# Kernel tuning notes

Measured on AMD Instinct MI355X. Metric: run time of the kernel, lower is better.

## Reference

```python
import jax, jax.numpy as jnp
import numpy as np

B, L, C, H, W = 2, 8, 64, 128, 128
HID = 256


def setup_inputs() -> dict:
    key = jax.random.key(0)
    k0, k1, k2, k3, k4 = jax.random.split(key, 5)
    x = jax.random.normal(k0, (B, L, C, H, W), dtype=jnp.float32)
    # Conv2d(in*4 -> hidden, kernel=1): weight stored as [out, in] for 1x1
    conv_w = jax.random.normal(k1, (HID, 4 * C), dtype=jnp.float32) * (1.0 / np.sqrt(4 * C))
    conv_b = jax.random.normal(k2, (HID,), dtype=jnp.float32) * 0.01
    conv_out_w = jax.random.normal(k3, (4 * C, HID), dtype=jnp.float32) * (1.0 / np.sqrt(HID))
    conv_out_b = jax.random.normal(k4, (4 * C,), dtype=jnp.float32) * 0.01
    return {"x": x, "conv_w": conv_w, "conv_b": conv_b,
            "conv_out_w": conv_out_w, "conv_out_b": conv_out_b}


def _dwt(x):  # x: [N, C, Hp, Wp] (even dims) -> [N, 4C, Hp/2, Wp/2]
    x1 = x[:, :, 0::2, 0::2] * 0.5
    x2 = x[:, :, 1::2, 0::2] * 0.5
    x3 = x[:, :, 0::2, 1::2] * 0.5
    x4 = x[:, :, 1::2, 1::2] * 0.5
    return jnp.concatenate([x1 + x2 + x3 + x4,
                            -x1 - x2 + x3 + x4,
                            -x1 + x2 - x3 + x4,
                            x1 - x2 - x3 + x4], axis=1)


def _idwt(y):  # y: [N, 4C, Hh, Wh] -> [N, C, 2Hh, 2Wh]
    n, c4, hh, wh = y.shape
    co = c4 // 4
    y1 = y[:, 0 * co:1 * co] * 0.5
    y2 = y[:, 1 * co:2 * co] * 0.5
    y3 = y[:, 2 * co:3 * co] * 0.5
    y4 = y[:, 3 * co:4 * co] * 0.5
    a = y1 - y2 - y3 + y4   # h[0::2, 0::2]
    b = y1 - y2 + y3 - y4   # h[1::2, 0::2]
    c = y1 + y2 - y3 - y4   # h[0::2, 1::2]
    d = y1 + y2 + y3 + y4   # h[1::2, 1::2]
    r0 = jnp.stack([a, c], axis=-1).reshape(n, co, hh, 2 * wh)  # even rows
    r1 = jnp.stack([b, d], axis=-1).reshape(n, co, hh, 2 * wh)  # odd rows
    return jnp.stack([r0, r1], axis=-2).reshape(n, co, 2 * hh, 2 * wh)


def reference(x, conv_w, conv_b, conv_out_w, conv_out_b):
    b, l, c, h, w = x.shape
    pad_h = (2 - h % 2) % 2
    pad_w = (2 - w % 2) % 2
    if pad_h > 0 or pad_w > 0:
        x = jnp.pad(x, ((0, 0), (0, 0), (0, 0), (0, pad_h), (0, pad_w)))
    hp, wp = x.shape[-2], x.shape[-1]
    xf = x.reshape(b * l, c, hp, wp)
    x_dwt = _dwt(xf)                                       # [BL, 4C, hp/2, wp/2]
    feat = jnp.einsum('nchw,oc->nohw', x_dwt, conv_w) + conv_b[None, :, None, None]
    feat = jax.nn.silu(feat)
    y = jnp.einsum('nchw,oc->nohw', feat, conv_out_w) + conv_out_b[None, :, None, None]
    rec = _idwt(y)                                         # [BL, C, hp, wp]
    out = rec.reshape(b, l, c, hp, wp)
    if pad_h > 0 or pad_w > 0:
        out = out[..., :h, :w]
    return out
```

## Files before the change

### kernel.cpp

```cpp
#include <hip/hip_runtime.h>
#include <hip/hip_bf16.h>


typedef __bf16 bf16x8 __attribute__((ext_vector_type(8)));
typedef float  f32x4  __attribute__((ext_vector_type(4)));

#define SP 264

__device__ __forceinline__ unsigned short f2bf(float f) {
  __hip_bfloat16 h = __float2bfloat16(f);
  return __builtin_bit_cast(unsigned short, h);
}
__device__ __forceinline__ float bf2f(unsigned short s) {
  union { unsigned int i; float f; } v; v.i = ((unsigned int)s) << 16; return v.f;
}
__device__ __forceinline__ float silu(float f) {
  return f / (1.0f + __expf(-f));
}
__device__ __forceinline__ bf16x8 ldw8(const float* __restrict__ p) {
  const float4 a = *(const float4*)p;
  const float4 b = *(const float4*)(p + 4);
  bf16x8 r;
  r[0] = (__bf16)a.x; r[1] = (__bf16)a.y; r[2] = (__bf16)a.z; r[3] = (__bf16)a.w;
  r[4] = (__bf16)b.x; r[5] = (__bf16)b.y; r[6] = (__bf16)b.z; r[7] = (__bf16)b.w;
  return r;
}

__global__ __launch_bounds__(256) void cvt_w(const float* __restrict__ w1,
                                             const float* __restrict__ w2,
                                             unsigned short* __restrict__ o) {
  const int i = (blockIdx.x * 256 + threadIdx.x) * 4;
  const float4 a = *(const float4*)(w1 + i);
  const float4 b = *(const float4*)(w2 + i);
  *(ushort4*)(o + i)         = make_ushort4(f2bf(a.x), f2bf(a.y), f2bf(a.z), f2bf(a.w));
  *(ushort4*)(o + 65536 + i) = make_ushort4(f2bf(b.x), f2bf(b.y), f2bf(b.z), f2bf(b.w));
}

template <bool WBF16>
__global__ __launch_bounds__(256, 4)
void wavelet_fused(const float* __restrict__ x,
                   const void* __restrict__ w1p,
                   const float* __restrict__ b1,
                   const void* __restrict__ w2p,
                   const float* __restrict__ b2,
                   float* __restrict__ out)
{
  __shared__ unsigned short lds[64 * SP];

  const int t  = threadIdx.x;
  const int n  = blockIdx.x >> 6;
  const int hh = blockIdx.x & 63;

  const int ww = t & 63;
  const int cg = t >> 6;

  {
    const float* xb = x + ((size_t)n * 64 * 128 + (size_t)(2 * hh)) * 128 + 2 * ww;
    #pragma unroll
    for (int j = 0; j < 4; ++j) {
      const int c0 = (cg + 4 * j) * 4;
      float qv[4][4];
      #pragma unroll
      for (int ci = 0; ci < 4; ++ci) {
        const float* p = xb + (size_t)(c0 + ci) * (128 * 128);
        const float2 r0 = *(const float2*)p;
        const float2 r1 = *(const float2*)(p + 128);
        const float x1 = r0.x, x3 = r0.y;
        const float x2 = r1.x, x4 = r1.y;
        qv[0][ci] = 0.5f * ((x1 + x2) + (x3 + x4));
        qv[1][ci] = 0.5f * ((x3 + x4) - (x1 + x2));
        qv[2][ci] = 0.5f * ((x2 + x4) - (x1 + x3));
        qv[3][ci] = 0.5f * ((x1 + x4) - (x2 + x3));
      }
      #pragma unroll
      for (int q = 0; q < 4; ++q) {
        ushort4 v = make_ushort4(f2bf(qv[q][0]), f2bf(qv[q][1]), f2bf(qv[q][2]), f2bf(qv[q][3]));
        *(ushort4*)(&lds[ww * SP + q * 64 + c0]) = v;
      }
    }
  }
  __syncthreads();

  const int wv   = t >> 6;
  const int r    = t & 15;
  const int quad = (t & 63) >> 4;

  {
    f32x4 acc[4][4];
    #pragma unroll
    for (int mt = 0; mt < 4; ++mt)
      #pragma unroll
      for (int nt = 0; nt < 4; ++nt)
        acc[mt][nt] = (f32x4){0.0f, 0.0f, 0.0f, 0.0f};

    #pragma unroll
    for (int k0 = 0; k0 < 256; k0 += 32) {
      bf16x8 a[4], b[4];
      #pragma unroll
      for (int mt = 0; mt < 4; ++mt) {
        const int row = wv * 64 + mt * 16 + r;
        if constexpr (WBF16)
          a[mt] = *(const bf16x8*)((const unsigned short*)w1p + row * 256 + quad * 8 + k0);
        else
          a[mt] = ldw8((const float*)w1p + row * 256 + quad * 8 + k0);
      }
      #pragma unroll
      for (int nt = 0; nt < 4; ++nt)
        b[nt] = *(const bf16x8*)(&lds[(nt * 16 + r) * SP + quad * 8 + k0]);
      #pragma unroll
      for (int mt = 0; mt < 4; ++mt)
        #pragma unroll
        for (int nt = 0; nt < 4; ++nt)
          acc[mt][nt] = __builtin_amdgcn_mfma_f32_16x16x32_bf16(a[mt], b[nt], acc[mt][nt], 0, 0, 0);
    }
    __syncthreads();

    #pragma unroll
    for (int mt = 0; mt < 4; ++mt) {
      const int ob = wv * 64 + mt * 16 + quad * 4;
      const float4 bb = *(const float4*)(b1 + ob);
      #pragma unroll
      for (int nt = 0; nt < 4; ++nt) {
        const int pix = nt * 16 + r;
        ushort4 v;
        v.x = f2bf(silu(acc[mt][nt][0] + bb.x));
        v.y = f2bf(silu(acc[mt][nt][1] + bb.y));
        v.z = f2bf(silu(acc[mt][nt][2] + bb.z));
        v.w = f2bf(silu(acc[mt][nt][3] + bb.w));
        *(ushort4*)(&lds[pix * SP + ob]) = v;
      }
    }
  }
  __syncthreads();

  {
    f32x4 acc[4][4];
    #pragma unroll
    for (int mt = 0; mt < 4; ++mt)
      #pragma unroll
      for (int nt = 0; nt < 4; ++nt)
        acc[mt][nt] = (f32x4){0.0f, 0.0f, 0.0f, 0.0f};

    #pragma unroll
    for (int k0 = 0; k0 < 256; k0 += 32) {
      bf16x8 a[4], b[4];
      #pragma unroll
      for (int mt = 0; mt < 4; ++mt) {
        const int row = wv * 64 + mt * 16 + r;
        if constexpr (WBF16)
          a[mt] = *(const bf16x8*)((const unsigned short*)w2p + row * 256 + quad * 8 + k0);
        else
          a[mt] = ldw8((const float*)w2p + row * 256 + quad * 8 + k0);
      }
      #pragma unroll
      for (int nt = 0; nt < 4; ++nt)
        b[nt] = *(const bf16x8*)(&lds[(nt * 16 + r) * SP + quad * 8 + k0]);
      #pragma unroll
      for (int mt = 0; mt < 4; ++mt)
        #pragma unroll
        for (int nt = 0; nt < 4; ++nt)
          acc[mt][nt] = __builtin_amdgcn_mfma_f32_16x16x32_bf16(a[mt], b[nt], acc[mt][nt], 0, 0, 0);
    }
    __syncthreads();

    #pragma unroll
    for (int mt = 0; mt < 4; ++mt) {
      const int cb = wv * 64 + mt * 16 + quad * 4;
      const float4 bb = *(const float4*)(b2 + cb);
      #pragma unroll
      for (int nt = 0; nt < 4; ++nt) {
        const int pix = nt * 16 + r;
        ushort4 v;
        v.x = f2bf(acc[mt][nt][0] + bb.x);
        v.y = f2bf(acc[mt][nt][1] + bb.y);
        v.z = f2bf(acc[mt][nt][2] + bb.z);
        v.w = f2bf(acc[mt][nt][3] + bb.w);
        *(ushort4*)(&lds[pix * SP + cb]) = v;
      }
    }
  }
  __syncthreads();

  {
    float* ob_ = out + ((size_t)n * 64 * 128 + (size_t)(2 * hh)) * 128 + 2 * ww;
    #pragma unroll
    for (int j = 0; j < 4; ++j) {
      const int c0 = (cg + 4 * j) * 4;
      unsigned short yb[4][4];
      #pragma unroll
      for (int q = 0; q < 4; ++q) {
        const ushort4 v = *(const ushort4*)(&lds[ww * SP + q * 64 + c0]);
        yb[q][0] = v.x; yb[q][1] = v.y; yb[q][2] = v.z; yb[q][3] = v.w;
      }
      #pragma unroll
      for (int ci = 0; ci < 4; ++ci) {
        const float y1 = 0.5f * bf2f(yb[0][ci]);
        const float y2 = 0.5f * bf2f(yb[1][ci]);
        const float y3 = 0.5f * bf2f(yb[2][ci]);
        const float y4 = 0.5f * bf2f(yb[3][ci]);
        const float s14 = y1 + y4, s23 = y2 + y3;
        const float d14 = y1 - y4, d23 = y2 - y3;
        const float oa  = s14 - s23;
        const float oc  = d14 + d23;
        const float obv = d14 - d23;
        const float od  = s14 + s23;
        float* prow = ob_ + (size_t)(c0 + ci) * (128 * 128);
        *(float2*)prow         = make_float2(oa, oc);
        *(float2*)(prow + 128) = make_float2(obv, od);
      }
    }
  }
}

extern "C" void kernel_launch(void* const* d_in, const int* in_sizes, int n_in,
                              void* d_out, int out_size, void* d_ws, size_t ws_size,
                              hipStream_t stream) {
  (void)in_sizes; (void)n_in; (void)out_size;
  const float* x  = (const float*)d_in[0];
  const float* w1 = (const float*)d_in[1];
  const float* b1 = (const float*)d_in[2];
  const float* w2 = (const float*)d_in[3];
  const float* b2 = (const float*)d_in[4];
  float* o = (float*)d_out;

  if (ws_size >= 2u * 65536u * sizeof(unsigned short)) {
    unsigned short* wb = (unsigned short*)d_ws;
    cvt_w<<<dim3(64), dim3(256), 0, stream>>>(w1, w2, wb);
    wavelet_fused<true><<<dim3(16 * 64), dim3(256), 0, stream>>>(
        x, wb, b1, wb + 65536, b2, o);
  } else {
    wavelet_fused<false><<<dim3(16 * 64), dim3(256), 0, stream>>>(
        x, w1, b1, w2, b2, o);
  }
}
```

Before: 154.8 us.

## Split blocks to half-rows, switch to 32x32x16 MFMA, batch input loads

Each block now covers 32 half-row pixels with 128 threads (two waves, each computing 128 output channels) instead of 64 pixels with 256 threads, which doubles the grid and halves the LDS footprint. The GEMMs switch from 16x16x32 to 32x32x16 bf16 MFMA, so each wave issues 4 larger MFMAs per k-step with a single shared B fragment. All input float2 loads are issued up front into registers before the DWT math so more memory requests are in flight. The cost is more weight-fragment traffic per pixel, since each block reloads the full weights for half as many pixels, plus higher register pressure from the batched loads.

```diff
diff --git a/kernel.cpp b/kernel.cpp
--- a/kernel.cpp
+++ b/kernel.cpp
@@ -2,8 +2,8 @@
 #include <hip/hip_bf16.h>
 
 
-typedef __bf16 bf16x8 __attribute__((ext_vector_type(8)));
-typedef float  f32x4  __attribute__((ext_vector_type(4)));
+typedef __bf16 bf16x8  __attribute__((ext_vector_type(8)));
+typedef float  f32x16  __attribute__((ext_vector_type(16)));
 
 #define SP 264
 
@@ -37,7 +37,7 @@
 }
 
 template <bool WBF16>
-__global__ __launch_bounds__(256, 4)
+__global__ __launch_bounds__(128, 4)
 void wavelet_fused(const float* __restrict__ x,
                    const void* __restrict__ w1p,
                    const float* __restrict__ b1,
@@ -45,28 +45,37 @@
                    const float* __restrict__ b2,
                    float* __restrict__ out)
 {
-  __shared__ unsigned short lds[64 * SP];
-
-  const int t  = threadIdx.x;
-  const int n  = blockIdx.x >> 6;
-  const int hh = blockIdx.x & 63;
-
-  const int ww = t & 63;
-  const int cg = t >> 6;
-
-  {
-    const float* xb = x + ((size_t)n * 64 * 128 + (size_t)(2 * hh)) * 128 + 2 * ww;
+  __shared__ unsigned short lds[32 * SP];
+
+  const int t    = threadIdx.x;
+  const int bid  = blockIdx.x;
+  const int n    = bid >> 7;
+  const int hh   = (bid >> 1) & 63;
+  const int half = bid & 1;
+
+  const int ww  = t & 31;
+  const int cg  = t >> 5;
+  const int col = half * 32 + ww;
+
+  {
+    float2 r0v[16], r1v[16];
+    #pragma unroll
+    for (int j = 0; j < 4; ++j)
+      #pragma unroll
+      for (int ci = 0; ci < 4; ++ci) {
+        const int c = (cg + 4 * j) * 4 + ci;
+        const float* p = x + ((size_t)(n * 64 + c) * 128 + (size_t)(2 * hh)) * 128 + 2 * col;
+        r0v[j * 4 + ci] = *(const float2*)p;
+        r1v[j * 4 + ci] = *(const float2*)(p + 128);
+      }
     #pragma unroll
     for (int j = 0; j < 4; ++j) {
       const int c0 = (cg + 4 * j) * 4;
       float qv[4][4];
       #pragma unroll
       for (int ci = 0; ci < 4; ++ci) {
-        const float* p = xb + (size_t)(c0 + ci) * (128 * 128);
-        const float2 r0 = *(const float2*)p;
-        const float2 r1 = *(const float2*)(p + 128);
-        const float x1 = r0.x, x3 = r0.y;
-        const float x2 = r1.x, x4 = r1.y;
+        const float x1 = r0v[j * 4 + ci].x, x3 = r0v[j * 4 + ci].y;
+        const float x2 = r1v[j * 4 + ci].x, x4 = r1v[j * 4 + ci].y;
         qv[0][ci] = 0.5f * ((x1 + x2) + (x3 + x4));
         qv[1][ci] = 0.5f * ((x3 + x4) - (x1 + x2));
         qv[2][ci] = 0.5f * ((x2 + x4) - (x1 + x3));
@@ -81,108 +90,95 @@
   }
   __syncthreads();
 
-  const int wv   = t >> 6;
-  const int r    = t & 15;
-  const int quad = (t & 63) >> 4;
-
-  {
-    f32x4 acc[4][4];
+  const int wv    = t >> 6;
+  const int lane  = t & 63;
+  const int m     = lane & 31;
+  const int khalf = lane >> 5;
+
+  {
+    f32x16 acc[4];
     #pragma unroll
     for (int mt = 0; mt < 4; ++mt)
-      #pragma unroll
-      for (int nt = 0; nt < 4; ++nt)
-        acc[mt][nt] = (f32x4){0.0f, 0.0f, 0.0f, 0.0f};
-
-    #pragma unroll
-    for (int k0 = 0; k0 < 256; k0 += 32) {
-      bf16x8 a[4], b[4];
+      acc[mt] = (f32x16)(0.0f);
+
+    #pragma unroll
+    for (int k0 = 0; k0 < 256; k0 += 16) {
+      bf16x8 a[4], b;
       #pragma unroll
       for (int mt = 0; mt < 4; ++mt) {
-        const int row = wv * 64 + mt * 16 + r;
+        const int row = wv * 128 + mt * 32 + m;
         if constexpr (WBF16)
-          a[mt] = *(const bf16x8*)((const unsigned short*)w1p + row * 256 + quad * 8 + k0);
+          a[mt] = *(const bf16x8*)((const unsigned short*)w1p + row * 256 + k0 + khalf * 8);
         else
-          a[mt] = ldw8((const float*)w1p + row * 256 + quad * 8 + k0);
-      }
-      #pragma unroll
-      for (int nt = 0; nt < 4; ++nt)
-        b[nt] = *(const bf16x8*)(&lds[(nt * 16 + r) * SP + quad * 8 + k0]);
+          a[mt] = ldw8((const float*)w1p + row * 256 + k0 + khalf * 8);
+      }
+      b = *(const bf16x8*)(&lds[m * SP + k0 + khalf * 8]);
       #pragma unroll
       for (int mt = 0; mt < 4; ++mt)
-        #pragma unroll
-        for (int nt = 0; nt < 4; ++nt)
-          acc[mt][nt] = __builtin_amdgcn_mfma_f32_16x16x32_bf16(a[mt], b[nt], acc[mt][nt], 0, 0, 0);
+        acc[mt] = __builtin_amdgcn_mfma_f32_32x32x16_bf16(a[mt], b, acc[mt], 0, 0, 0);
     }
     __syncthreads();
 
     #pragma unroll
     for (int mt = 0; mt < 4; ++mt) {
-      const int ob = wv * 64 + mt * 16 + quad * 4;
-      const float4 bb = *(const float4*)(b1 + ob);
-      #pragma unroll
-      for (int nt = 0; nt < 4; ++nt) {
-        const int pix = nt * 16 + r;
+      #pragma unroll
+      for (int g = 0; g < 4; ++g) {
+        const int o = wv * 128 + mt * 32 + g * 8 + khalf * 4;
+        const float4 bb = *(const float4*)(b1 + o);
         ushort4 v;
-        v.x = f2bf(silu(acc[mt][nt][0] + bb.x));
-        v.y = f2bf(silu(acc[mt][nt][1] + bb.y));
-        v.z = f2bf(silu(acc[mt][nt][2] + bb.z));
-        v.w = f2bf(silu(acc[mt][nt][3] + bb.w));
-        *(ushort4*)(&lds[pix * SP + ob]) = v;
+        v.x = f2bf(silu(acc[mt][g * 4 + 0] + bb.x));
+        v.y = f2bf(silu(acc[mt][g * 4 + 1] + bb.y));
+        v.z = f2bf(silu(acc[mt][g * 4 + 2] + bb.z));
+        v.w = f2bf(silu(acc[mt][g * 4 + 3] + bb.w));
+        *(ushort4*)(&lds[m * SP + o]) = v;
       }
     }
   }
   __syncthreads();
 
   {
-    f32x4 acc[4][4];
+    f32x16 acc[4];
     #pragma unroll
     for (int mt = 0; mt < 4; ++mt)
-      #pragma unroll
-      for (int nt = 0; nt < 4; ++nt)
-        acc[mt][nt] = (f32x4){0.0f, 0.0f, 0.0f, 0.0f};
-
-    #pragma unroll
-    for (int k0 = 0; k0 < 256; k0 += 32) {
-      bf16x8 a[4], b[4];
+      acc[mt] = (f32x16)(0.0f);
+
+    #pragma unroll
+    for (int k0 = 0; k0 < 256; k0 += 16) {
+      bf16x8 a[4], b;
       #pragma unroll
       for (int mt = 0; mt < 4; ++mt) {
-        const int row = wv * 64 + mt * 16 + r;
+        const int row = wv * 128 + mt * 32 + m;
         if constexpr (WBF16)
-          a[mt] = *(const bf16x8*)((const unsigned short*)w2p + row * 256 + quad * 8 + k0);
+          a[mt] = *(const bf16x8*)((const unsigned short*)w2p + row * 256 + k0 + khalf * 8);
         else
-          a[mt] = ldw8((const float*)w2p + row * 256 + quad * 8 + k0);
-      }
-      #pragma unroll
-      for (int nt = 0; nt < 4; ++nt)
-        b[nt] = *(const bf16x8*)(&lds[(nt * 16 + r) * SP + quad * 8 + k0]);
+          a[mt] = ldw8((const float*)w2p + row * 256 + k0 + khalf * 8);
+      }
+      b = *(const bf16x8*)(&lds[m * SP + k0 + khalf * 8]);
       #pragma unroll
       for (int mt = 0; mt < 4; ++mt)
-        #pragma unroll
-        for (int nt = 0; nt < 4; ++nt)
-          acc[mt][nt] = __builtin_amdgcn_mfma_f32_16x16x32_bf16(a[mt], b[nt], acc[mt][nt], 0, 0, 0);
+        acc[mt] = __builtin_amdgcn_mfma_f32_32x32x16_bf16(a[mt], b, acc[mt], 0, 0, 0);
     }
     __syncthreads();
 
     #pragma unroll
     for (int mt = 0; mt < 4; ++mt) {
-      const int cb = wv * 64 + mt * 16 + quad * 4;
-      const float4 bb = *(const float4*)(b2 + cb);
-      #pragma unroll
-      for (int nt = 0; nt < 4; ++nt) {
-        const int pix = nt * 16 + r;
+      #pragma unroll
+      for (int g = 0; g < 4; ++g) {
+        const int cb = wv * 128 + mt * 32 + g * 8 + khalf * 4;
+        const float4 bb = *(const float4*)(b2 + cb);
         ushort4 v;
-        v.x = f2bf(acc[mt][nt][0] + bb.x);
-        v.y = f2bf(acc[mt][nt][1] + bb.y);
-        v.z = f2bf(acc[mt][nt][2] + bb.z);
-        v.w = f2bf(acc[mt][nt][3] + bb.w);
-        *(ushort4*)(&lds[pix * SP + cb]) = v;
+        v.x = f2bf(acc[mt][g * 4 + 0] + bb.x);
+        v.y = f2bf(acc[mt][g * 4 + 1] + bb.y);
+        v.z = f2bf(acc[mt][g * 4 + 2] + bb.z);
+        v.w = f2bf(acc[mt][g * 4 + 3] + bb.w);
+        *(ushort4*)(&lds[m * SP + cb]) = v;
       }
     }
   }
   __syncthreads();
 
   {
-    float* ob_ = out + ((size_t)n * 64 * 128 + (size_t)(2 * hh)) * 128 + 2 * ww;
+    float* ob_ = out + ((size_t)n * 64 * 128 + (size_t)(2 * hh)) * 128 + 2 * col;
     #pragma unroll
     for (int j = 0; j < 4; ++j) {
       const int c0 = (cg + 4 * j) * 4;
@@ -226,10 +222,10 @@
   if (ws_size >= 2u * 65536u * sizeof(unsigned short)) {
     unsigned short* wb = (unsigned short*)d_ws;
     cvt_w<<<dim3(64), dim3(256), 0, stream>>>(w1, w2, wb);
-    wavelet_fused<true><<<dim3(16 * 64), dim3(256), 0, stream>>>(
+    wavelet_fused<true><<<dim3(16 * 64 * 2), dim3(128), 0, stream>>>(
         x, wb, b1, wb + 65536, b2, o);
   } else {
-    wavelet_fused<false><<<dim3(16 * 64), dim3(256), 0, stream>>>(
+    wavelet_fused<false><<<dim3(16 * 64 * 2), dim3(128), 0, stream>>>(
         x, w1, b1, w2, b2, o);
   }
 }
```

After: 180.7 us. 1.17x slower.

## Prefetch weight fragments, batch input loads, and XOR-swizzle LDS layout

Applied to the files above, without the earlier changes.

Issues all input x loads up front, then computes the wavelet transform from registers. The weight fragments for the next k-step are loaded into registers one step ahead, and the loads carry over from the first GEMM into the second, so global latency overlaps the MFMA work. The padded LDS stride is replaced by an XOR swizzle on 256-wide rows, which shrinks LDS use to 32 KB while keeping accesses free of bank conflicts. The extra live registers from the batched loads and double-buffered fragments may reduce occupancy.

```diff
diff --git a/kernel.cpp b/kernel.cpp
--- a/kernel.cpp
+++ b/kernel.cpp
@@ -4,8 +4,6 @@
 
 typedef __bf16 bf16x8 __attribute__((ext_vector_type(8)));
 typedef float  f32x4  __attribute__((ext_vector_type(4)));
-
-#define SP 264
 
 __device__ __forceinline__ unsigned short f2bf(float f) {
   __hip_bfloat16 h = __float2bfloat16(f);
@@ -16,6 +14,9 @@
 }
 __device__ __forceinline__ float silu(float f) {
   return f / (1.0f + __expf(-f));
+}
+__device__ __forceinline__ int sw(int pix, int k) {
+  return pix * 256 + ((((k >> 3) ^ pix) & 31) << 3) + (k & 7);
 }
 __device__ __forceinline__ bf16x8 ldw8(const float* __restrict__ p) {
   const float4 a = *(const float4*)p;
@@ -45,7 +46,7 @@
                    const float* __restrict__ b2,
                    float* __restrict__ out)
 {
-  __shared__ unsigned short lds[64 * SP];
+  __shared__ unsigned short lds[64 * 256];
 
   const int t  = threadIdx.x;
   const int n  = blockIdx.x >> 6;
@@ -54,19 +55,41 @@
   const int ww = t & 63;
   const int cg = t >> 6;
 
+  const int wv   = t >> 6;
+  const int r    = t & 15;
+  const int quad = (t & 63) >> 4;
+
+  const unsigned short* w1b16 = (const unsigned short*)w1p + (wv * 64 + r) * 256 + quad * 8;
+  const unsigned short* w2b16 = (const unsigned short*)w2p + (wv * 64 + r) * 256 + quad * 8;
+  const float*          w1b32 = (const float*)w1p + (wv * 64 + r) * 256 + quad * 8;
+  const float*          w2b32 = (const float*)w2p + (wv * 64 + r) * 256 + quad * 8;
+
+  bf16x8 a_cur[4], a_nxt[4];
+
   {
     const float* xb = x + ((size_t)n * 64 * 128 + (size_t)(2 * hh)) * 128 + 2 * ww;
+    float2 r0v[16], r1v[16];
+    #pragma unroll
+    for (int j = 0; j < 4; ++j)
+      #pragma unroll
+      for (int ci = 0; ci < 4; ++ci) {
+        const float* p = xb + (size_t)((cg + 4 * j) * 4 + ci) * (128 * 128);
+        r0v[j * 4 + ci] = *(const float2*)p;
+        r1v[j * 4 + ci] = *(const float2*)(p + 128);
+      }
+    #pragma unroll
+    for (int mt = 0; mt < 4; ++mt)
+      a_cur[mt] = WBF16 ? *(const bf16x8*)(w1b16 + mt * (16 * 256))
+                        : ldw8(w1b32 + mt * (16 * 256));
+
     #pragma unroll
     for (int j = 0; j < 4; ++j) {
       const int c0 = (cg + 4 * j) * 4;
       float qv[4][4];
       #pragma unroll
       for (int ci = 0; ci < 4; ++ci) {
-        const float* p = xb + (size_t)(c0 + ci) * (128 * 128);
-        const float2 r0 = *(const float2*)p;
-        const float2 r1 = *(const float2*)(p + 128);
-        const float x1 = r0.x, x3 = r0.y;
-        const float x2 = r1.x, x4 = r1.y;
+        const float x1 = r0v[j * 4 + ci].x, x3 = r0v[j * 4 + ci].y;
+        const float x2 = r1v[j * 4 + ci].x, x4 = r1v[j * 4 + ci].y;
         qv[0][ci] = 0.5f * ((x1 + x2) + (x3 + x4));
         qv[1][ci] = 0.5f * ((x3 + x4) - (x1 + x2));
         qv[2][ci] = 0.5f * ((x2 + x4) - (x1 + x3));
@@ -75,16 +98,12 @@
       #pragma unroll
       for (int q = 0; q < 4; ++q) {
         ushort4 v = make_ushort4(f2bf(qv[q][0]), f2bf(qv[q][1]), f2bf(qv[q][2]), f2bf(qv[q][3]));
-        *(ushort4*)(&lds[ww * SP + q * 64 + c0]) = v;
+        *(ushort4*)(&lds[sw(ww, q * 64 + c0)]) = v;
       }
     }
   }
   __syncthreads();
 
-  const int wv   = t >> 6;
-  const int r    = t & 15;
-  const int quad = (t & 63) >> 4;
-
   {
     f32x4 acc[4][4];
     #pragma unroll
@@ -95,23 +114,27 @@
 
     #pragma unroll
     for (int k0 = 0; k0 < 256; k0 += 32) {
-      bf16x8 a[4], b[4];
       #pragma unroll
       for (int mt = 0; mt < 4; ++mt) {
-        const int row = wv * 64 + mt * 16 + r;
-        if constexpr (WBF16)
-          a[mt] = *(const bf16x8*)((const unsigned short*)w1p + row * 256 + quad * 8 + k0);
+        if (k0 < 224)
+          a_nxt[mt] = WBF16 ? *(const bf16x8*)(w1b16 + mt * (16 * 256) + k0 + 32)
+                            : ldw8(w1b32 + mt * (16 * 256) + k0 + 32);
         else
-          a[mt] = ldw8((const float*)w1p + row * 256 + quad * 8 + k0);
-      }
-      #pragma unroll
-      for (int nt = 0; nt < 4; ++nt)
-        b[nt] = *(const bf16x8*)(&lds[(nt * 16 + r) * SP + quad * 8 + k0]);
+          a_nxt[mt] = WBF16 ? *(const bf16x8*)(w2b16 + mt * (16 * 256))
+                            : ldw8(w2b32 + mt * (16 * 256));
+      }
+      bf16x8 b[4];
+      #pragma unroll
+      for (int nt = 0; nt < 4; ++nt)
+        b[nt] = *(const bf16x8*)(&lds[sw(nt * 16 + r, quad * 8 + k0)]);
       #pragma unroll
       for (int mt = 0; mt < 4; ++mt)
         #pragma unroll
         for (int nt = 0; nt < 4; ++nt)
-          acc[mt][nt] = __builtin_amdgcn_mfma_f32_16x16x32_bf16(a[mt], b[nt], acc[mt][nt], 0, 0, 0);
+          acc[mt][nt] = __builtin_amdgcn_mfma_f32_16x16x32_bf16(a_cur[mt], b[nt], acc[mt][nt], 0, 0, 0);
+      #pragma unroll
+      for (int mt = 0; mt < 4; ++mt)
+        a_cur[mt] = a_nxt[mt];
     }
     __syncthreads();
 
@@ -127,7 +150,7 @@
         v.y = f2bf(silu(acc[mt][nt][1] + bb.y));
         v.z = f2bf(silu(acc[mt][nt][2] + bb.z));
         v.w = f2bf(silu(acc[mt][nt][3] + bb.w));
-        *(ushort4*)(&lds[pix * SP + ob]) = v;
+        *(ushort4*)(&lds[sw(pix, ob)]) = v;
       }
     }
   }
@@ -143,23 +166,24 @@
 
     #pragma unroll
     for (int k0 = 0; k0 < 256; k0 += 32) {
-      bf16x8 a[4], b[4];
-      #pragma unroll
-      for (int mt = 0; mt < 4; ++mt) {
-        const int row = wv * 64 + mt * 16 + r;
-        if constexpr (WBF16)
-          a[mt] = *(const bf16x8*)((const unsigned short*)w2p + row * 256 + quad * 8 + k0);
-        else
-          a[mt] = ldw8((const float*)w2p + row * 256 + quad * 8 + k0);
-      }
-      #pragma unroll
-      for (int nt = 0; nt < 4; ++nt)
-        b[nt] = *(const bf16x8*)(&lds[(nt * 16 + r) * SP + quad * 8 + k0]);
+      #pragma unroll
+      for (int mt = 0; mt < 4; ++mt)
+        if (k0 < 224)
+          a_nxt[mt] = WBF16 ? *(const bf16x8*)(w2b16 + mt * (16 * 256) + k0 + 32)
+                            : ldw8(w2b32 + mt * (16 * 256) + k0 + 32);
+      bf16x8 b[4];
+      #pragma unroll
+      for (int nt = 0; nt < 4; ++nt)
+        b[nt] = *(const bf16x8*)(&lds[sw(nt * 16 + r, quad * 8 + k0)]);
       #pragma unroll
       for (int mt = 0; mt < 4; ++mt)
         #pragma unroll
         for (int nt = 0; nt < 4; ++nt)
-          acc[mt][nt] = __builtin_amdgcn_mfma_f32_16x16x32_bf16(a[mt], b[nt], acc[mt][nt], 0, 0, 0);
+          acc[mt][nt] = __builtin_amdgcn_mfma_f32_16x16x32_bf16(a_cur[mt], b[nt], acc[mt][nt], 0, 0, 0);
+      if (k0 < 224)
+        #pragma unroll
+        for (int mt = 0; mt < 4; ++mt)
+          a_cur[mt] = a_nxt[mt];
     }
     __syncthreads();
 
@@ -175,7 +199,7 @@
         v.y = f2bf(acc[mt][nt][1] + bb.y);
         v.z = f2bf(acc[mt][nt][2] + bb.z);
         v.w = f2bf(acc[mt][nt][3] + bb.w);
-        *(ushort4*)(&lds[pix * SP + cb]) = v;
+        *(ushort4*)(&lds[sw(pix, cb)]) = v;
       }
     }
   }
@@ -189,7 +213,7 @@
       unsigned short yb[4][4];
       #pragma unroll
       for (int q = 0; q < 4; ++q) {
-        const ushort4 v = *(const ushort4*)(&lds[ww * SP + q * 64 + c0]);
+        const ushort4 v = *(const ushort4*)(&lds[sw(ww, q * 64 + c0)]);
         yb[q][0] = v.x; yb[q][1] = v.y; yb[q][2] = v.z; yb[q][3] = v.w;
       }
       #pragma unroll
```

After: 165.9 us. 1.07x slower.
